# Performance work log

Measured on AMD Instinct MI355X. Metric: run time of the kernel, lower is better.

## Reference

```python
import jax, jax.numpy as jnp
import numpy as np
from jax.ops import segment_sum

N_NODES = 100000


def _deg_inv_sqrt(idx, n):
    # DGL GraphConv norm='both': degs clamped to min 1, then deg^{-0.5}
    deg = segment_sum(jnp.ones_like(idx, dtype=jnp.float32), idx, num_segments=n)
    return jnp.where(deg > 0, jax.lax.rsqrt(jnp.maximum(deg, 1.0)), 1.0)


def _graph_conv(x, src, dst, W, b, out_norm, in_norm, n):
    # norm='both': scale src feats by out_deg^-1/2, sum-aggregate, scale by in_deg^-1/2
    h = (x * out_norm[:, None]) @ W          # apply weight first (cheaper/equal width)
    msg = h[src]                              # [E, d] irregular gather
    agg = segment_sum(msg, dst, num_segments=n)
    return agg * in_norm[:, None] + b


def setup_inputs() -> dict:
    key = jax.random.key(0)
    k1, k2, k3, k4, k5, k6, k7 = jax.random.split(key, 7)
    E = 1600000
    in_feats, h_feats, out_feats = 128, 128, 64
    in_feat = jax.random.normal(k1, (N_NODES, in_feats), dtype=jnp.float32)
    src = jax.random.randint(k2, (E,), 0, N_NODES, dtype=jnp.int32)
    dst = jax.random.randint(k3, (E,), 0, N_NODES, dtype=jnp.int32)
    # Glorot-style init like dgl GraphConv
    W1 = jax.random.normal(k4, (in_feats, h_feats), dtype=jnp.float32) * (1.0 / np.sqrt(in_feats))
    b1 = jnp.zeros((h_feats,), dtype=jnp.float32)
    W2 = jax.random.normal(k5, (h_feats, out_feats), dtype=jnp.float32) * (1.0 / np.sqrt(h_feats))
    b2 = jnp.zeros((out_feats,), dtype=jnp.float32)
    return {"in_feat": in_feat, "src": src, "dst": dst, "W1": W1, "b1": b1, "W2": W2, "b2": b2}


def reference(in_feat, src, dst, W1, b1, W2, b2):
    n = in_feat.shape[0]
    out_norm = _deg_inv_sqrt(src, n)  # out-degree norm (source side)
    in_norm = _deg_inv_sqrt(dst, n)   # in-degree norm (destination side)
    h = _graph_conv(in_feat, src, dst, W1, b1, out_norm, in_norm, n)
    z = jax.nn.relu(h)
    h2 = _graph_conv(z, src, dst, W2, b2, out_norm, in_norm, n)
    return (h2, z)
```

## Files before the change

kernel.cpp:

```cpp
#include <hip/hip_runtime.h>

#define N_NODES 100000
#define N_EDGES 1600000
#define NB 391
#define BCAP 5120
#define PART_BLOCKS 250
#define EPB 6400
#define GSTRIDE 16

typedef __attribute__((ext_vector_type(8))) short short8;
typedef __attribute__((ext_vector_type(4))) float f32x4;

__device__ inline unsigned short f2bf(float f) {
    unsigned int u = __builtin_bit_cast(unsigned int, f);
    u += 0x7fffu + ((u >> 16) & 1u);
    return (unsigned short)(u >> 16);
}
__device__ inline float bf2f(unsigned short h) {
    unsigned int u = ((unsigned int)h) << 16;
    return __builtin_bit_cast(float, u);
}

__global__ __launch_bounds__(1024) void k_part(const int* __restrict__ src, const int* __restrict__ dst,
                                               int* __restrict__ gcurD, int* __restrict__ gcurS,
                                               unsigned int* __restrict__ ebuf,
                                               unsigned char* __restrict__ ebufS,
                                               const float* __restrict__ W1, const float* __restrict__ W2,
                                               unsigned short* __restrict__ Wp1, unsigned short* __restrict__ Wp2) {
    if (blockIdx.x >= PART_BLOCKS) {
        int i = (blockIdx.x - PART_BLOCKS) * 1024 + threadIdx.x;
        if (i < 2048) {
            int kq = i >> 7, c = i & 127;
#pragma unroll
            for (int j = 0; j < 8; j++) Wp1[i * 8 + j] = f2bf(W1[(kq * 8 + j) * 128 + c]);
        } else if (i < 3072) {
            int i2 = i - 2048;
            int kq = i2 >> 6, c = i2 & 63;
#pragma unroll
            for (int j = 0; j < 8; j++) Wp2[i2 * 8 + j] = f2bf(W2[(kq * 8 + j) * 64 + c]);
        }
        return;
    }
    __shared__ uint2 est[EPB];
    __shared__ unsigned int sortedPk[EPB];
    __shared__ unsigned short bIdD[EPB];
    __shared__ unsigned short bIdS[EPB];
    __shared__ unsigned char sByte[EPB];
    __shared__ int histD[NB], histS[NB], startD[NB], startS[NB];
    __shared__ int gbD[NB], gbS[NB], cursD[NB], cursS[NB];
    __shared__ int s1[256];
    int t = threadIdx.x;
    for (int i = t; i < NB; i += 1024) { histD[i] = 0; histS[i] = 0; }
    __syncthreads();
    int base = blockIdx.x * EPB;
    for (int i = t; i < EPB; i += 1024) {
        int s = src[base + i], d = dst[base + i];
        est[i] = make_uint2((unsigned int)s, (unsigned int)d);
        atomicAdd(&histD[d >> 8], 1);
        atomicAdd(&histS[s >> 8], 1);
    }
    __syncthreads();
    for (int i = t; i < NB; i += 1024) {
        int hD = histD[i], hS = histS[i];
        gbD[i] = hD ? atomicAdd(&gcurD[i * GSTRIDE], hD) : 0;
        gbS[i] = hS ? atomicAdd(&gcurS[i * GSTRIDE], hS) : 0;
    }
    if (t < 256) {
        int a = (2 * t < NB) ? histD[2 * t] : 0;
        int b = (2 * t + 1 < NB) ? histD[2 * t + 1] : 0;
        s1[t] = a + b;
    }
    __syncthreads();
    for (int o = 1; o < 256; o <<= 1) {
        int v = 0;
        if (t < 256) v = s1[t] + (t >= o ? s1[t - o] : 0);
        __syncthreads();
        if (t < 256) s1[t] = v;
        __syncthreads();
    }
    if (t < 256) {
        int excl = (t > 0) ? s1[t - 1] : 0;
        if (2 * t < NB) { startD[2 * t] = excl; cursD[2 * t] = excl; }
        if (2 * t + 1 < NB) {
            int e2 = excl + histD[2 * t];
            startD[2 * t + 1] = e2; cursD[2 * t + 1] = e2;
        }
    }
    __syncthreads();
    if (t < 256) {
        int a = (2 * t < NB) ? histS[2 * t] : 0;
        int b = (2 * t + 1 < NB) ? histS[2 * t + 1] : 0;
        s1[t] = a + b;
    }
    __syncthreads();
    for (int o = 1; o < 256; o <<= 1) {
        int v = 0;
        if (t < 256) v = s1[t] + (t >= o ? s1[t - o] : 0);
        __syncthreads();
        if (t < 256) s1[t] = v;
        __syncthreads();
    }
    if (t < 256) {
        int excl = (t > 0) ? s1[t - 1] : 0;
        if (2 * t < NB) { startS[2 * t] = excl; cursS[2 * t] = excl; }
        if (2 * t + 1 < NB) {
            int e2 = excl + histS[2 * t];
            startS[2 * t + 1] = e2; cursS[2 * t + 1] = e2;
        }
    }
    __syncthreads();
    for (int i = t; i < EPB; i += 1024) {
        uint2 e2 = est[i];
        int s = (int)e2.x, d = (int)e2.y;
        int bd = d >> 8;
        int r = atomicAdd(&cursD[bd], 1);
        sortedPk[r] = ((unsigned int)s << 8) | (unsigned int)(d & 255);
        bIdD[r] = (unsigned short)bd;
        int bs = s >> 8;
        int r2 = atomicAdd(&cursS[bs], 1);
        sByte[r2] = (unsigned char)(s & 255);
        bIdS[r2] = (unsigned short)bs;
    }
    __syncthreads();
    for (int i = t; i < EPB; i += 1024) {
        int b = bIdD[i];
        int pos = gbD[b] + (i - startD[b]);
        if (pos < BCAP) ebuf[(size_t)b * BCAP + pos] = sortedPk[i];
        int b2 = bIdS[i];
        int pos2 = gbS[b2] + (i - startS[b2]);
        if (pos2 < BCAP) ebufS[(size_t)b2 * BCAP + pos2] = sByte[i];
    }
}

__global__ __launch_bounds__(256) void k_bhist_scan(const unsigned char* __restrict__ ebufS,
                                                    const int* __restrict__ gcurS,
                                                    float* __restrict__ out_norm,
                                                    const int* __restrict__ gcurD,
                                                    int* __restrict__ bbase, int* __restrict__ row_ptr) {
    int t = threadIdx.x;
    if (blockIdx.x < NB) {
        __shared__ int hist[256];
        int b = blockIdx.x;
        hist[t] = 0;
        __syncthreads();
        int ne = min(gcurS[b * GSTRIDE], BCAP);
        const unsigned char* eb = ebufS + (size_t)b * BCAP;
        int nv = ne >> 2;
        const uchar4* ev = (const uchar4*)eb;
        for (int i = t; i < nv; i += 256) {
            uchar4 u = ev[i];
            atomicAdd(&hist[u.x], 1); atomicAdd(&hist[u.y], 1);
            atomicAdd(&hist[u.z], 1); atomicAdd(&hist[u.w], 1);
        }
        for (int i = (nv << 2) + t; i < ne; i += 256) atomicAdd(&hist[eb[i]], 1);
        __syncthreads();
        int node = b * 256 + t;
        if (node < N_NODES) out_norm[node] = hist[t] > 0 ? rsqrtf((float)hist[t]) : 1.0f;
    } else {
        __shared__ int s[NB + 1];
        for (int i = t; i < NB; i += 256) s[i] = min(gcurD[i * GSTRIDE], BCAP);
        __syncthreads();
        if (t == 0) {
            int run = 0;
            for (int b = 0; b < NB; b++) { int v = s[b]; s[b] = run; run += v; }
            s[NB] = run;
        }
        __syncthreads();
        for (int i = t; i < NB + 1; i += 256) bbase[i] = s[i];
        if (t == 0) row_ptr[N_NODES] = s[NB];
    }
}

__global__ __launch_bounds__(256) void k_bsort_xb(const unsigned int* __restrict__ ebuf, const int* __restrict__ gcurD,
                                                  const int* __restrict__ bbase, int* __restrict__ csr_src,
                                                  int* __restrict__ row_ptr, float* __restrict__ in_norm,
                                                  const float* __restrict__ x, const float* __restrict__ out_norm,
                                                  unsigned short* __restrict__ xb) {
    __shared__ int perm[BCAP];
    __shared__ int hist[256], cursor[256], sa[256], sb[256];
    int t = threadIdx.x;
    if (blockIdx.x >= NB) {
        int tid = (blockIdx.x - NB) * 256 + t;
        int row = tid >> 5;
        float4 v = ((const float4*)x)[tid];
        float w = out_norm[row];
        unsigned int lo = (unsigned int)f2bf(v.x * w) | ((unsigned int)f2bf(v.y * w) << 16);
        unsigned int hi = (unsigned int)f2bf(v.z * w) | ((unsigned int)f2bf(v.w * w) << 16);
        ((uint2*)xb)[tid] = make_uint2(lo, hi);
        return;
    }
    int b = blockIdx.x;
    int ne = min(gcurD[b * GSTRIDE], BCAP);
    const unsigned int* eb = ebuf + (size_t)b * BCAP;
    hist[t] = 0;
    __syncthreads();
    for (int i = t; i < ne; i += 256) atomicAdd(&hist[eb[i] & 255u], 1);
    __syncthreads();
    sa[t] = hist[t];
    __syncthreads();
    int* cur = sa; int* nxt = sb;
    for (int o = 1; o < 256; o <<= 1) {
        int v = cur[t] + (t >= o ? cur[t - o] : 0);
        nxt[t] = v;
        __syncthreads();
        int* tmp = cur; cur = nxt; nxt = tmp;
    }
    int ex = cur[t] - hist[t];
    cursor[t] = ex;
    int node = b * 256 + t;
    if (node < N_NODES) {
        row_ptr[node] = bbase[b] + ex;
        in_norm[node] = hist[t] > 0 ? rsqrtf((float)hist[t]) : 1.0f;
    }
    __syncthreads();
    for (int i = t; i < ne; i += 256) {
        unsigned int pk = eb[i];
        int pos = atomicAdd(&cursor[pk & 255u], 1);
        perm[pos] = (int)(pk >> 8);
    }
    __syncthreads();
    int gb = bbase[b];
    for (int i = t; i < ne; i += 256) csr_src[gb + i] = perm[i];
}

__global__ __launch_bounds__(256) void k_agg1(const unsigned short* __restrict__ xb,
                                              const int* __restrict__ row_ptr, const int* __restrict__ csr,
                                              const float* __restrict__ in_norm,
                                              unsigned short* __restrict__ aggb) {
    int wave = threadIdx.x >> 6, lane = threadIdx.x & 63;
    int d = blockIdx.x * 4 + wave;
    if (d >= N_NODES) return;
    int e0 = __builtin_amdgcn_readfirstlane(row_ptr[d]);
    int e1 = __builtin_amdgcn_readfirstlane(row_ptr[d + 1]);
    int col = lane << 1;
    float accL[8], accH[8];
#pragma unroll
    for (int j = 0; j < 8; j++) { accL[j] = 0.f; accH[j] = 0.f; }
    int e = e0;
    for (; e + 8 <= e1; e += 8) {
        int sI[8];
#pragma unroll
        for (int j = 0; j < 8; j++) sI[j] = __builtin_amdgcn_readfirstlane(csr[e + j]);
        unsigned int v[8];
#pragma unroll
        for (int j = 0; j < 8; j++) v[j] = *(const unsigned int*)(xb + (size_t)sI[j] * 128 + col);
#pragma unroll
        for (int j = 0; j < 8; j++) {
            accL[j] += bf2f((unsigned short)(v[j] & 0xffffu));
            accH[j] += bf2f((unsigned short)(v[j] >> 16));
        }
    }
    if (e + 4 <= e1) {
        int sI[4];
#pragma unroll
        for (int j = 0; j < 4; j++) sI[j] = __builtin_amdgcn_readfirstlane(csr[e + j]);
        unsigned int v[4];
#pragma unroll
        for (int j = 0; j < 4; j++) v[j] = *(const unsigned int*)(xb + (size_t)sI[j] * 128 + col);
#pragma unroll
        for (int j = 0; j < 4; j++) {
            accL[j] += bf2f((unsigned short)(v[j] & 0xffffu));
            accH[j] += bf2f((unsigned short)(v[j] >> 16));
        }
        e += 4;
    }
    if (e + 2 <= e1) {
        int sI[2];
#pragma unroll
        for (int j = 0; j < 2; j++) sI[j] = __builtin_amdgcn_readfirstlane(csr[e + j]);
        unsigned int v[2];
#pragma unroll
        for (int j = 0; j < 2; j++) v[j] = *(const unsigned int*)(xb + (size_t)sI[j] * 128 + col);
#pragma unroll
        for (int j = 0; j < 2; j++) {
            accL[j] += bf2f((unsigned short)(v[j] & 0xffffu));
            accH[j] += bf2f((unsigned short)(v[j] >> 16));
        }
        e += 2;
    }
    if (e < e1) {
        int s = __builtin_amdgcn_readfirstlane(csr[e]);
        unsigned int v = *(const unsigned int*)(xb + (size_t)s * 128 + col);
        accL[0] += bf2f((unsigned short)(v & 0xffffu));
        accH[0] += bf2f((unsigned short)(v >> 16));
    }
    float a0 = 0.f, a1 = 0.f;
#pragma unroll
    for (int j = 0; j < 8; j++) { a0 += accL[j]; a1 += accH[j]; }
    float w = in_norm[d];
    unsigned int pk = (unsigned int)f2bf(a0 * w) | ((unsigned int)f2bf(a1 * w) << 16);
    *(unsigned int*)(aggb + (size_t)d * 128 + col) = pk;
}

__global__ __launch_bounds__(256) void k_gemm12(const unsigned short* __restrict__ Ab,
                                                const unsigned short* __restrict__ Wp1,
                                                const unsigned short* __restrict__ Wp2,
                                                const float* __restrict__ bias1,
                                                const float* __restrict__ out_norm,
                                                float* __restrict__ z_out,
                                                unsigned short* __restrict__ tb) {
    __shared__ __align__(16) unsigned short zt[64 * 132];
    int wave = threadIdx.x >> 6, lane = threadIdx.x & 63;
    int base = (blockIdx.x * 4 + wave) * 16;
    if (base >= N_NODES) return;
    int m = lane & 15, q = lane >> 4;
    short8 a[4];
#pragma unroll
    for (int t = 0; t < 4; t++) a[t] = *(const short8*)(Ab + (size_t)(base + m) * 128 + t * 32 + q * 8);
    f32x4 acc[8];
#pragma unroll
    for (int c = 0; c < 8; c++) acc[c] = (f32x4)(0.f);
#pragma unroll
    for (int ct = 0; ct < 8; ct++) {
#pragma unroll
        for (int t = 0; t < 4; t++) {
            short8 b = *(const short8*)(Wp1 + ((size_t)((t * 4 + q) * 128 + ct * 16 + m)) * 8);
            acc[ct] = __builtin_amdgcn_mfma_f32_16x16x32_bf16(a[t], b, acc[ct], 0, 0, 0);
        }
    }
    float onr[4];
#pragma unroll
    for (int i = 0; i < 4; i++) onr[i] = out_norm[base + q * 4 + i];
#pragma unroll
    for (int ct = 0; ct < 8; ct++) {
        int col = ct * 16 + m;
        float bv = bias1[col];
#pragma unroll
        for (int i = 0; i < 4; i++) {
            int row = base + q * 4 + i;
            float v = acc[ct][i] + bv;
            v = v > 0.f ? v : 0.f;
            z_out[(size_t)row * 128 + col] = v;
            zt[(wave * 16 + q * 4 + i) * 132 + col] = f2bf(v * onr[i]);
        }
    }
    short8 a2[4];
#pragma unroll
    for (int t = 0; t < 4; t++) a2[t] = *(const short8*)(zt + (wave * 16 + m) * 132 + t * 32 + q * 8);
    f32x4 acc2[4];
#pragma unroll
    for (int c = 0; c < 4; c++) acc2[c] = (f32x4)(0.f);
#pragma unroll
    for (int ct = 0; ct < 4; ct++) {
#pragma unroll
        for (int t = 0; t < 4; t++) {
            short8 b = *(const short8*)(Wp2 + ((size_t)((t * 4 + q) * 64 + ct * 16 + m)) * 8);
            acc2[ct] = __builtin_amdgcn_mfma_f32_16x16x32_bf16(a2[t], b, acc2[ct], 0, 0, 0);
        }
    }
#pragma unroll
    for (int ct = 0; ct < 4; ct++) {
        int col = ct * 16 + m;
#pragma unroll
        for (int i = 0; i < 4; i++) {
            int row = base + q * 4 + i;
            tb[(size_t)row * 64 + col] = f2bf(acc2[ct][i]);
        }
    }
}

__global__ __launch_bounds__(256) void k_agg2(const unsigned short* __restrict__ tb,
                                              const int* __restrict__ row_ptr, const int* __restrict__ csr,
                                              const float* __restrict__ in_norm, const float* __restrict__ b2,
                                              float* __restrict__ out_h2) {
    int wave = threadIdx.x >> 6, lane = threadIdx.x & 63;
    int half = lane >> 5, li = lane & 31;
    int d = blockIdx.x * 4 + wave;
    if (d >= N_NODES) return;
    int e0 = __builtin_amdgcn_readfirstlane(row_ptr[d]);
    int e1 = __builtin_amdgcn_readfirstlane(row_ptr[d + 1]);
    int col = li << 1;
    float accA[8], accB[8];
#pragma unroll
    for (int j = 0; j < 8; j++) { accA[j] = 0.f; accB[j] = 0.f; }
    int e = e0;
    for (; e + 16 <= e1; e += 16) {
        int sI[8];
#pragma unroll
        for (int j = 0; j < 8; j++) {
            int sA = __builtin_amdgcn_readfirstlane(csr[e + 2 * j]);
            int sB = __builtin_amdgcn_readfirstlane(csr[e + 2 * j + 1]);
            sI[j] = half ? sB : sA;
        }
        unsigned int v[8];
#pragma unroll
        for (int j = 0; j < 8; j++) v[j] = *(const unsigned int*)(tb + (size_t)sI[j] * 64 + col);
#pragma unroll
        for (int j = 0; j < 8; j++) {
            accA[j] += bf2f((unsigned short)(v[j] & 0xffffu));
            accB[j] += bf2f((unsigned short)(v[j] >> 16));
        }
    }
    if (e + 8 <= e1) {
        int sI[4];
#pragma unroll
        for (int j = 0; j < 4; j++) {
            int sA = __builtin_amdgcn_readfirstlane(csr[e + 2 * j]);
            int sB = __builtin_amdgcn_readfirstlane(csr[e + 2 * j + 1]);
            sI[j] = half ? sB : sA;
        }
        unsigned int v[4];
#pragma unroll
        for (int j = 0; j < 4; j++) v[j] = *(const unsigned int*)(tb + (size_t)sI[j] * 64 + col);
#pragma unroll
        for (int j = 0; j < 4; j++) {
            accA[j] += bf2f((unsigned short)(v[j] & 0xffffu));
            accB[j] += bf2f((unsigned short)(v[j] >> 16));
        }
        e += 8;
    }
    if (e + 4 <= e1) {
        int sI[2];
#pragma unroll
        for (int j = 0; j < 2; j++) {
            int sA = __builtin_amdgcn_readfirstlane(csr[e + 2 * j]);
            int sB = __builtin_amdgcn_readfirstlane(csr[e + 2 * j + 1]);
            sI[j] = half ? sB : sA;
        }
        unsigned int v[2];
#pragma unroll
        for (int j = 0; j < 2; j++) v[j] = *(const unsigned int*)(tb + (size_t)sI[j] * 64 + col);
#pragma unroll
        for (int j = 0; j < 2; j++) {
            accA[j] += bf2f((unsigned short)(v[j] & 0xffffu));
            accB[j] += bf2f((unsigned short)(v[j] >> 16));
        }
        e += 2 * 2;
    }
    if (e + 2 <= e1) {
        int sA = __builtin_amdgcn_readfirstlane(csr[e]);
        int sB = __builtin_amdgcn_readfirstlane(csr[e + 1]);
        int s = half ? sB : sA;
        unsigned int v = *(const unsigned int*)(tb + (size_t)s * 64 + col);
        accA[0] += bf2f((unsigned short)(v & 0xffffu));
        accB[0] += bf2f((unsigned short)(v >> 16));
        e += 2;
    }
    if (e < e1) {
        int s = __builtin_amdgcn_readfirstlane(csr[e]);
        unsigned int v = *(const unsigned int*)(tb + (size_t)s * 64 + col);
        if (half == 0) {
            accA[0] += bf2f((unsigned short)(v & 0xffffu));
            accB[0] += bf2f((unsigned short)(v >> 16));
        }
    }
    float a0 = 0.f, a1 = 0.f;
#pragma unroll
    for (int j = 0; j < 8; j++) { a0 += accA[j]; a1 += accB[j]; }
    a0 += __shfl_xor(a0, 32);
    a1 += __shfl_xor(a1, 32);
    if (half == 0) {
        float w = in_norm[d];
        float2 r;
        r.x = a0 * w + b2[col];
        r.y = a1 * w + b2[col + 1];
        *(float2*)(out_h2 + (size_t)d * 64 + col) = r;
    }
}

extern "C" void kernel_launch(void* const* d_in, const int* in_sizes, int n_in,
                              void* d_out, int out_size, void* d_ws, size_t ws_size,
                              hipStream_t stream) {
    const float* x   = (const float*)d_in[0];
    const int*   src = (const int*)d_in[1];
    const int*   dst = (const int*)d_in[2];
    const float* W1  = (const float*)d_in[3];
    const float* b1  = (const float*)d_in[4];
    const float* W2  = (const float*)d_in[5];
    const float* b2  = (const float*)d_in[6];
    float* out_h2 = (float*)d_out;
    float* out_z  = (float*)d_out + N_NODES * 64;

    char* ws = (char*)d_ws;
    size_t off = 0;
    auto alloc = [&](size_t bytes) -> char* {
        char* p = ws + off;
        off = (off + bytes + 255) & ~(size_t)255;
        return p;
    };
    int* gcurD    = (int*)alloc(NB * GSTRIDE * 4);
    int* gcurS    = (int*)alloc(NB * GSTRIDE * 4);
    int* bbase    = (int*)alloc((NB + 1) * 4);
    int* row_ptr  = (int*)alloc((N_NODES + 1) * 4);
    float* out_norm = (float*)alloc(N_NODES * 4);
    float* in_norm  = (float*)alloc(N_NODES * 4);
    unsigned int* ebuf = (unsigned int*)alloc((size_t)NB * BCAP * 4);
    unsigned char* ebufS = (unsigned char*)alloc((size_t)NB * BCAP);
    int* csr_src  = (int*)alloc((size_t)N_EDGES * 4);
    unsigned short* Wp1 = (unsigned short*)alloc(2048 * 8 * 2);
    unsigned short* Wp2 = (unsigned short*)alloc(1024 * 8 * 2);
    unsigned short* xb    = (unsigned short*)alloc((size_t)N_NODES * 128 * 2);
    unsigned short* agg1b = (unsigned short*)alloc((size_t)N_NODES * 128 * 2);
    unsigned short* tb    = (unsigned short*)alloc((size_t)N_NODES * 64 * 2);
    (void)ws_size; (void)in_sizes; (void)n_in; (void)out_size;

    const size_t gcur_pad = ((size_t)(NB * GSTRIDE * 4) + 255) & ~(size_t)255;
    hipMemsetAsync(gcurD, 0, gcur_pad + (size_t)NB * GSTRIDE * 4, stream);

    const int GD_AGG = (N_NODES + 3) / 4;
    const int GD_GEMM = (N_NODES / 16 + 3) / 4;
    const int GD_XB = N_NODES * 32 / 256;

    k_part<<<PART_BLOCKS + 3, 1024, 0, stream>>>(src, dst, gcurD, gcurS, ebuf, ebufS, W1, W2, Wp1, Wp2);
    k_bhist_scan<<<NB + 1, 256, 0, stream>>>(ebufS, gcurS, out_norm, gcurD, bbase, row_ptr);
    k_bsort_xb<<<NB + GD_XB, 256, 0, stream>>>(ebuf, gcurD, bbase, csr_src, row_ptr, in_norm, x, out_norm, xb);
    k_agg1<<<GD_AGG, 256, 0, stream>>>(xb, row_ptr, csr_src, in_norm, agg1b);
    k_gemm12<<<GD_GEMM, 256, 0, stream>>>(agg1b, Wp1, Wp2, b1, out_norm, out_z, tb);
    k_agg2<<<GD_AGG, 256, 0, stream>>>(tb, row_ptr, csr_src, in_norm, b2, out_h2);
}
```

Baseline: 276.9 us.

## Merge histogram, scan and sort kernels; apply source norm during aggregation

Combines the out-degree histogram, the bucket prefix scan and the dst bucket sort plus bf16 conversion into one launch. Each sort block now computes its own bucket base by reducing the earlier buckets' counts, which removes the separate scan kernel and the bbase array. Because out_norm is no longer ready when x is converted, the source normalization moves into agg1 as an extra per-edge scalar load and an FMA. This saves one kernel launch and its dependency barrier, at the cost of redundant prefix reductions per block and extra gathers of out_norm.

```diff
diff --git a/kernel.cpp b/kernel.cpp
--- a/kernel.cpp
+++ b/kernel.cpp
@@ -132,15 +132,28 @@
     }
 }
 
-__global__ __launch_bounds__(256) void k_bhist_scan(const unsigned char* __restrict__ ebufS,
-                                                    const int* __restrict__ gcurS,
-                                                    float* __restrict__ out_norm,
-                                                    const int* __restrict__ gcurD,
-                                                    int* __restrict__ bbase, int* __restrict__ row_ptr) {
+__global__ __launch_bounds__(256) void k_bsort_bhist_xb(const unsigned int* __restrict__ ebuf,
+                                                        const int* __restrict__ gcurD,
+                                                        int* __restrict__ csr_src,
+                                                        int* __restrict__ row_ptr, float* __restrict__ in_norm,
+                                                        const unsigned char* __restrict__ ebufS,
+                                                        const int* __restrict__ gcurS,
+                                                        float* __restrict__ out_norm,
+                                                        const float* __restrict__ x,
+                                                        unsigned short* __restrict__ xb) {
+    __shared__ int perm[BCAP];
+    __shared__ int hist[256], cursor[256], sa[256], sb[256];
     int t = threadIdx.x;
-    if (blockIdx.x < NB) {
-        __shared__ int hist[256];
-        int b = blockIdx.x;
+    if (blockIdx.x >= 2 * NB) {
+        int tid = (blockIdx.x - 2 * NB) * 256 + t;
+        float4 v = ((const float4*)x)[tid];
+        unsigned int lo = (unsigned int)f2bf(v.x) | ((unsigned int)f2bf(v.y) << 16);
+        unsigned int hi = (unsigned int)f2bf(v.z) | ((unsigned int)f2bf(v.w) << 16);
+        ((uint2*)xb)[tid] = make_uint2(lo, hi);
+        return;
+    }
+    if (blockIdx.x >= NB) {
+        int b = blockIdx.x - NB;
         hist[t] = 0;
         __syncthreads();
         int ne = min(gcurS[b * GSTRIDE], BCAP);
@@ -156,42 +169,21 @@
         __syncthreads();
         int node = b * 256 + t;
         if (node < N_NODES) out_norm[node] = hist[t] > 0 ? rsqrtf((float)hist[t]) : 1.0f;
-    } else {
-        __shared__ int s[NB + 1];
-        for (int i = t; i < NB; i += 256) s[i] = min(gcurD[i * GSTRIDE], BCAP);
-        __syncthreads();
-        if (t == 0) {
-            int run = 0;
-            for (int b = 0; b < NB; b++) { int v = s[b]; s[b] = run; run += v; }
-            s[NB] = run;
-        }
-        __syncthreads();
-        for (int i = t; i < NB + 1; i += 256) bbase[i] = s[i];
-        if (t == 0) row_ptr[N_NODES] = s[NB];
-    }
-}
-
-__global__ __launch_bounds__(256) void k_bsort_xb(const unsigned int* __restrict__ ebuf, const int* __restrict__ gcurD,
-                                                  const int* __restrict__ bbase, int* __restrict__ csr_src,
-                                                  int* __restrict__ row_ptr, float* __restrict__ in_norm,
-                                                  const float* __restrict__ x, const float* __restrict__ out_norm,
-                                                  unsigned short* __restrict__ xb) {
-    __shared__ int perm[BCAP];
-    __shared__ int hist[256], cursor[256], sa[256], sb[256];
-    int t = threadIdx.x;
-    if (blockIdx.x >= NB) {
-        int tid = (blockIdx.x - NB) * 256 + t;
-        int row = tid >> 5;
-        float4 v = ((const float4*)x)[tid];
-        float w = out_norm[row];
-        unsigned int lo = (unsigned int)f2bf(v.x * w) | ((unsigned int)f2bf(v.y * w) << 16);
-        unsigned int hi = (unsigned int)f2bf(v.z * w) | ((unsigned int)f2bf(v.w * w) << 16);
-        ((uint2*)xb)[tid] = make_uint2(lo, hi);
         return;
     }
     int b = blockIdx.x;
     int ne = min(gcurD[b * GSTRIDE], BCAP);
     const unsigned int* eb = ebuf + (size_t)b * BCAP;
+    int partial = 0;
+    for (int i = t; i < b; i += 256) partial += min(gcurD[i * GSTRIDE], BCAP);
+    sa[t] = partial;
+    __syncthreads();
+    for (int o = 128; o > 0; o >>= 1) {
+        if (t < o) sa[t] += sa[t + o];
+        __syncthreads();
+    }
+    int gb = sa[0];
+    __syncthreads();
     hist[t] = 0;
     __syncthreads();
     for (int i = t; i < ne; i += 256) atomicAdd(&hist[eb[i] & 255u], 1);
@@ -209,9 +201,10 @@
     cursor[t] = ex;
     int node = b * 256 + t;
     if (node < N_NODES) {
-        row_ptr[node] = bbase[b] + ex;
+        row_ptr[node] = gb + ex;
         in_norm[node] = hist[t] > 0 ? rsqrtf((float)hist[t]) : 1.0f;
     }
+    if (b == NB - 1 && t == 0) row_ptr[N_NODES] = gb + ne;
     __syncthreads();
     for (int i = t; i < ne; i += 256) {
         unsigned int pk = eb[i];
@@ -219,13 +212,12 @@
         perm[pos] = (int)(pk >> 8);
     }
     __syncthreads();
-    int gb = bbase[b];
     for (int i = t; i < ne; i += 256) csr_src[gb + i] = perm[i];
 }
 
 __global__ __launch_bounds__(256) void k_agg1(const unsigned short* __restrict__ xb,
                                               const int* __restrict__ row_ptr, const int* __restrict__ csr,
-                                              const float* __restrict__ in_norm,
+                                              const float* __restrict__ in_norm, const float* __restrict__ out_norm,
                                               unsigned short* __restrict__ aggb) {
     int wave = threadIdx.x >> 6, lane = threadIdx.x & 63;
     int d = blockIdx.x * 4 + wave;
@@ -241,26 +233,32 @@
         int sI[8];
 #pragma unroll
         for (int j = 0; j < 8; j++) sI[j] = __builtin_amdgcn_readfirstlane(csr[e + j]);
+        float w8[8];
+#pragma unroll
+        for (int j = 0; j < 8; j++) w8[j] = out_norm[sI[j]];
         unsigned int v[8];
 #pragma unroll
         for (int j = 0; j < 8; j++) v[j] = *(const unsigned int*)(xb + (size_t)sI[j] * 128 + col);
 #pragma unroll
         for (int j = 0; j < 8; j++) {
-            accL[j] += bf2f((unsigned short)(v[j] & 0xffffu));
-            accH[j] += bf2f((unsigned short)(v[j] >> 16));
+            accL[j] = fmaf(w8[j], bf2f((unsigned short)(v[j] & 0xffffu)), accL[j]);
+            accH[j] = fmaf(w8[j], bf2f((unsigned short)(v[j] >> 16)), accH[j]);
         }
     }
     if (e + 4 <= e1) {
         int sI[4];
 #pragma unroll
         for (int j = 0; j < 4; j++) sI[j] = __builtin_amdgcn_readfirstlane(csr[e + j]);
+        float w4[4];
+#pragma unroll
+        for (int j = 0; j < 4; j++) w4[j] = out_norm[sI[j]];
         unsigned int v[4];
 #pragma unroll
         for (int j = 0; j < 4; j++) v[j] = *(const unsigned int*)(xb + (size_t)sI[j] * 128 + col);
 #pragma unroll
         for (int j = 0; j < 4; j++) {
-            accL[j] += bf2f((unsigned short)(v[j] & 0xffffu));
-            accH[j] += bf2f((unsigned short)(v[j] >> 16));
+            accL[j] = fmaf(w4[j], bf2f((unsigned short)(v[j] & 0xffffu)), accL[j]);
+            accH[j] = fmaf(w4[j], bf2f((unsigned short)(v[j] >> 16)), accH[j]);
         }
         e += 4;
     }
@@ -268,21 +266,25 @@
         int sI[2];
 #pragma unroll
         for (int j = 0; j < 2; j++) sI[j] = __builtin_amdgcn_readfirstlane(csr[e + j]);
+        float w2[2];
+#pragma unroll
+        for (int j = 0; j < 2; j++) w2[j] = out_norm[sI[j]];
         unsigned int v[2];
 #pragma unroll
         for (int j = 0; j < 2; j++) v[j] = *(const unsigned int*)(xb + (size_t)sI[j] * 128 + col);
 #pragma unroll
         for (int j = 0; j < 2; j++) {
-            accL[j] += bf2f((unsigned short)(v[j] & 0xffffu));
-            accH[j] += bf2f((unsigned short)(v[j] >> 16));
+            accL[j] = fmaf(w2[j], bf2f((unsigned short)(v[j] & 0xffffu)), accL[j]);
+            accH[j] = fmaf(w2[j], bf2f((unsigned short)(v[j] >> 16)), accH[j]);
         }
         e += 2;
     }
     if (e < e1) {
         int s = __builtin_amdgcn_readfirstlane(csr[e]);
+        float w1 = out_norm[s];
         unsigned int v = *(const unsigned int*)(xb + (size_t)s * 128 + col);
-        accL[0] += bf2f((unsigned short)(v & 0xffffu));
-        accH[0] += bf2f((unsigned short)(v >> 16));
+        accL[0] = fmaf(w1, bf2f((unsigned short)(v & 0xffffu)), accL[0]);
+        accH[0] = fmaf(w1, bf2f((unsigned short)(v >> 16)), accH[0]);
     }
     float a0 = 0.f, a1 = 0.f;
 #pragma unroll
@@ -480,7 +482,6 @@
     };
     int* gcurD    = (int*)alloc(NB * GSTRIDE * 4);
     int* gcurS    = (int*)alloc(NB * GSTRIDE * 4);
-    int* bbase    = (int*)alloc((NB + 1) * 4);
     int* row_ptr  = (int*)alloc((N_NODES + 1) * 4);
     float* out_norm = (float*)alloc(N_NODES * 4);
     float* in_norm  = (float*)alloc(N_NODES * 4);
@@ -502,9 +503,9 @@
     const int GD_XB = N_NODES * 32 / 256;
 
     k_part<<<PART_BLOCKS + 3, 1024, 0, stream>>>(src, dst, gcurD, gcurS, ebuf, ebufS, W1, W2, Wp1, Wp2);
-    k_bhist_scan<<<NB + 1, 256, 0, stream>>>(ebufS, gcurS, out_norm, gcurD, bbase, row_ptr);
-    k_bsort_xb<<<NB + GD_XB, 256, 0, stream>>>(ebuf, gcurD, bbase, csr_src, row_ptr, in_norm, x, out_norm, xb);
-    k_agg1<<<GD_AGG, 256, 0, stream>>>(xb, row_ptr, csr_src, in_norm, agg1b);
+    k_bsort_bhist_xb<<<2 * NB + GD_XB, 256, 0, stream>>>(ebuf, gcurD, csr_src, row_ptr, in_norm,
+                                                         ebufS, gcurS, out_norm, x, xb);
+    k_agg1<<<GD_AGG, 256, 0, stream>>>(xb, row_ptr, csr_src, in_norm, out_norm, agg1b);
     k_gemm12<<<GD_GEMM, 256, 0, stream>>>(agg1b, Wp1, Wp2, b1, out_norm, out_z, tb);
     k_agg2<<<GD_AGG, 256, 0, stream>>>(tb, row_ptr, csr_src, in_norm, b2, out_h2);
 }
```

Result: no change. 272.3 us (-1.7%).
